# Optimization experiments

Hardware: AMD Instinct MI355X
Metric: run time of the kernel (lower is better)

## Reference

```python
import jax, jax.numpy as jnp
import numpy as np

N = 100000
D = 16          # input_dim
NUM_FILTERS = 8
NNZ = 1600000


def setup_inputs() -> dict:
    key = jax.random.key(0)
    k1, k2, k3, k4, k5 = jax.random.split(key, 5)
    x = jax.random.normal(k1, (N, D), dtype=jnp.float32)
    L_rows = jax.random.randint(k2, (NNZ,), 0, N, dtype=jnp.int64 if jax.config.jax_enable_x64 else jnp.int32).astype(jnp.int32)
    L_cols = jax.random.randint(k3, (NNZ,), 0, N, dtype=jnp.int32)
    L_v = jax.random.normal(k4, (NNZ,), dtype=jnp.float32)
    node_attr_eig = jax.random.uniform(k5, (N,), dtype=jnp.float32)
    return {"x": x, "L_rows": L_rows, "L_cols": L_cols, "L_v": L_v, "node_attr_eig": node_attr_eig}


def reference(x, L_rows, L_cols, L_v, node_attr_eig):
    n, d = x.shape
    f = NUM_FILTERS
    # exponents = 2 ** arange(num_filters + 1)
    exponents = (2 ** jnp.arange(f + 1)).astype(x.dtype)  # [F+1]
    # coeffs = x.T @ L  ==  (L.T @ x).T ; compute L.T @ x as [N, D]
    # (L.T @ x)[c] = sum over nnz entries (r, c): L_v * x[r]
    LTx = jax.ops.segment_sum(L_v[:, None] * x[L_rows], L_cols, num_segments=n)  # [N, D]
    # exponential eigenfilter bank: w = exp(-eig)^exponents, wavelet differences
    w = jnp.exp(-node_attr_eig)[:, None] ** exponents[None, :]  # [N, F+1]
    w_wav = w[:, :-1] - w[:, 1:]                                # [N, F]
    # g_eig = coeffs[..., None] * w_wav[None, ...] permuted to [N, D, F]
    g_eig = (LTx[:, :, None] * w_wav[:, None, :]).reshape(n, d * f)  # [N, D*F]
    # filtered = L @ g_eig : out[r] = sum over nnz (r, c): L_v * g_eig[c]
    out = jax.ops.segment_sum(L_v[:, None] * g_eig[L_cols], L_rows, num_segments=n)
    return out.reshape(n, d, f)
```

## Files before the change

kernel.cpp:

```cpp
#include <hip/hip_runtime.h>

#define N_NODES   100000
#define D_DIM     16
#define NFILT     8
#define KOUT      128
#define NNZ_CNT   1600000

#define CBITS     8
#define CROWS     256
#define NCB       ((N_NODES + CROWS - 1) / CROWS)
#define CAP       5120
#define EPB       4096
#define NBLKA     ((NNZ_CNT + EPB - 1) / EPB)

__device__ __forceinline__ uint f32_to_bf16_bits(float f) {
    uint u = __float_as_uint(f);
    uint r = (u + 0x7FFFu + ((u >> 16) & 1u)) >> 16;
    return r;
}

__global__ void wav_kernel(const float* __restrict__ eig, ushort* __restrict__ wavb) {
    int n = blockIdx.x * blockDim.x + threadIdx.x;
    if (n >= N_NODES) return;
    float cur = expf(-eig[n]);
    uint pk[4];
#pragma unroll
    for (int h = 0; h < 4; ++h) {
        float nx0 = cur * cur;
        float w0 = cur - nx0;
        float nx1 = nx0 * nx0;
        float w1 = nx0 - nx1;
        cur = nx1;
        pk[h] = f32_to_bf16_bits(w0) | (f32_to_bf16_bits(w1) << 16);
    }
    *(uint4*)(wavb + (size_t)n * NFILT) = make_uint4(pk[0], pk[1], pk[2], pk[3]);
}

__global__ __launch_bounds__(512) void binA_kernel(const int* __restrict__ keys,
                                                   const int* __restrict__ pays,
                                                   const float* __restrict__ v,
                                                   int* __restrict__ gcur,
                                                   int2* __restrict__ regA) {
    __shared__ int cnt[NCB];
    __shared__ int offb[NCB];
    __shared__ int gbase[NCB];
    __shared__ int sc[512];
    __shared__ int2 rec[EPB];
    int tid = threadIdx.x;
    int e0 = blockIdx.x * EPB;
    int nE = NNZ_CNT - e0; if (nE > EPB) nE = EPB;

    for (int i = tid; i < NCB; i += 512) cnt[i] = 0;
    __syncthreads();
    for (int i = tid; i < nE; i += 512)
        atomicAdd(&cnt[keys[e0 + i] >> CBITS], 1);
    __syncthreads();

    sc[tid] = (tid < NCB) ? cnt[tid] : 0;
    __syncthreads();
    for (int off = 1; off < 512; off <<= 1) {
        int t = (tid >= off) ? sc[tid - off] : 0;
        __syncthreads();
        sc[tid] += t;
        __syncthreads();
    }
    if (tid < NCB) {
        int cv = cnt[tid];
        int st = sc[tid] - cv;
        offb[tid] = st;
        gbase[tid] = cv ? atomicAdd(&gcur[tid], cv) : 0;
        cnt[tid] = st;
    }
    __syncthreads();

    for (int i = tid; i < nE; i += 512) {
        int k = keys[e0 + i], p = pays[e0 + i];
        float val = v[e0 + i];
        int b = k >> CBITS;
        int pos = atomicAdd(&cnt[b], 1);
        rec[pos] = make_int2(((k & (CROWS - 1)) << 17) | p, __float_as_int(val));
    }
    __syncthreads();

    int wv = tid >> 6, lane = tid & 63;
    for (int b = wv; b < NCB; b += 8) {
        int s = offb[b];
        int n = cnt[b] - s;
        size_t dst = (size_t)b * CAP + gbase[b];
        for (int i = lane; i < n; i += 64)
            regA[dst + i] = rec[s + i];
    }
}

__global__ __launch_bounds__(512) void binB_kernel(const int* __restrict__ gcur,
                                                   int2* __restrict__ regA,
                                                   int2* __restrict__ offs2) {
    __shared__ int2 rec[CAP];
    __shared__ int cnt[CROWS];
    __shared__ int sc[CROWS];
    int tid = threadIdx.x;
    int b = blockIdx.x;
    int nb = gcur[b]; if (nb > CAP) nb = CAP;
    size_t base = (size_t)b * CAP;

    if (tid < CROWS) cnt[tid] = 0;
    __syncthreads();
    for (int i = tid; i < nb; i += 512) {
        int2 r = regA[base + i];
        rec[i] = r;
        atomicAdd(&cnt[r.x >> 17], 1);
    }
    __syncthreads();

    int cv = (tid < CROWS) ? cnt[tid] : 0;
    if (tid < CROWS) sc[tid] = cv;
    __syncthreads();
    for (int off = 1; off < CROWS; off <<= 1) {
        int t = (tid < CROWS && tid >= off) ? sc[tid - off] : 0;
        __syncthreads();
        if (tid < CROWS) sc[tid] += t;
        __syncthreads();
    }
    if (tid < CROWS) {
        int st = sc[tid] - cv;
        int key = b * CROWS + tid;
        if (key < N_NODES)
            offs2[key] = make_int2((int)base + st, (int)base + st + cv);
        cnt[tid] = st;
    }
    __syncthreads();

    for (int i = tid; i < nb; i += 512) {
        int2 r = rec[i];
        int p = atomicAdd(&cnt[r.x >> 17], 1);
        regA[base + p] = make_int2(r.x & 0x1FFFF, r.y);
    }
}

__global__ __launch_bounds__(256) void gather1_kernel(const int2* __restrict__ offs2,
                                                      const int2* __restrict__ ep,
                                                      const float* __restrict__ x,
                                                      uint* __restrict__ LTxP) {
    int wave = (int)(((long long)blockIdx.x * blockDim.x + threadIdx.x) >> 6);
    if (wave >= N_NODES) return;
    int lane = threadIdx.x & 63;
    int c = wave;
    int d = lane & 15;
    int j = lane >> 4;
    int2 se = offs2[c];
    float acc = 0.f;
    for (int i = se.x + j; i < se.y; i += 4) {
        int2 e = ep[i];
        acc = fmaf(__int_as_float(e.y), x[(size_t)e.x * D_DIM + d], acc);
    }
    acc += __shfl_xor(acc, 16);
    acc += __shfl_xor(acc, 32);
    float hi = __shfl_down(acc, 8);
    if (lane < 8)
        LTxP[(size_t)c * NFILT + lane] = f32_to_bf16_bits(acc) | (f32_to_bf16_bits(hi) << 16);
}

__global__ __launch_bounds__(256) void gather2_kernel(const int2* __restrict__ offs2,
                                                      const int2* __restrict__ ep,
                                                      const uint* __restrict__ LTxP,
                                                      const ushort* __restrict__ wavb,
                                                      float* __restrict__ out) {
    int wave = (int)(((long long)blockIdx.x * blockDim.x + threadIdx.x) >> 6);
    if (wave >= N_NODES) return;
    int lane = threadIdx.x & 63;
    int r = wave;
    int d0 = lane >> 3;
    int f  = lane & 7;
    int2 se = offs2[r];
    int i = se.x, end = se.y;
    float acc0 = 0.f, acc1 = 0.f;
    for (; i + 4 <= end; i += 4) {
        int2 e0 = ep[i], e1 = ep[i + 1], e2 = ep[i + 2], e3 = ep[i + 3];
        uint l0 = LTxP[e0.x * NFILT + d0];
        uint l1 = LTxP[e1.x * NFILT + d0];
        uint l2 = LTxP[e2.x * NFILT + d0];
        uint l3 = LTxP[e3.x * NFILT + d0];
        uint w0 = wavb[e0.x * NFILT + f];
        uint w1 = wavb[e1.x * NFILT + f];
        uint w2 = wavb[e2.x * NFILT + f];
        uint w3 = wavb[e3.x * NFILT + f];
        float vw0 = __int_as_float(e0.y) * __uint_as_float(w0 << 16);
        float vw1 = __int_as_float(e1.y) * __uint_as_float(w1 << 16);
        float vw2 = __int_as_float(e2.y) * __uint_as_float(w2 << 16);
        float vw3 = __int_as_float(e3.y) * __uint_as_float(w3 << 16);
        acc0 = fmaf(vw0, __uint_as_float(l0 << 16), acc0);
        acc1 = fmaf(vw0, __uint_as_float(l0 & 0xFFFF0000u), acc1);
        acc0 = fmaf(vw1, __uint_as_float(l1 << 16), acc0);
        acc1 = fmaf(vw1, __uint_as_float(l1 & 0xFFFF0000u), acc1);
        acc0 = fmaf(vw2, __uint_as_float(l2 << 16), acc0);
        acc1 = fmaf(vw2, __uint_as_float(l2 & 0xFFFF0000u), acc1);
        acc0 = fmaf(vw3, __uint_as_float(l3 << 16), acc0);
        acc1 = fmaf(vw3, __uint_as_float(l3 & 0xFFFF0000u), acc1);
    }
    for (; i < end; ++i) {
        int2 e = ep[i];
        uint l = LTxP[e.x * NFILT + d0];
        uint w = wavb[e.x * NFILT + f];
        float vw = __int_as_float(e.y) * __uint_as_float(w << 16);
        acc0 = fmaf(vw, __uint_as_float(l << 16), acc0);
        acc1 = fmaf(vw, __uint_as_float(l & 0xFFFF0000u), acc1);
    }
    out[(size_t)r * KOUT + lane]      = acc0;
    out[(size_t)r * KOUT + 64 + lane] = acc1;
}

extern "C" void kernel_launch(void* const* d_in, const int* in_sizes, int n_in,
                              void* d_out, int out_size, void* d_ws, size_t ws_size,
                              hipStream_t stream) {
    const float* x      = (const float*)d_in[0];
    const int*   L_rows = (const int*)  d_in[1];
    const int*   L_cols = (const int*)  d_in[2];
    const float* L_v    = (const float*)d_in[3];
    const float* eig    = (const float*)d_in[4];
    float* out = (float*)d_out;

    uint*   LTxP  = (uint*)d_ws;
    ushort* wavb  = (ushort*)(LTxP + (size_t)N_NODES * NFILT);
    int2*   offs2 = (int2*)(wavb + (size_t)N_NODES * NFILT);
    int2*   regA  = offs2 + N_NODES;
    int*    gcur  = (int*)(regA + (size_t)NCB * CAP);
    int*    gcurB = gcur + NCB;

    hipMemsetAsync(gcur, 0, (size_t)2 * NCB * sizeof(int), stream);

    wav_kernel<<<(N_NODES + 255) / 256, 256, 0, stream>>>(eig, wavb);

    binA_kernel<<<NBLKA, 512, 0, stream>>>(L_cols, L_rows, L_v, gcurB, regA);
    binB_kernel<<<NCB, 512, 0, stream>>>(gcurB, regA, offs2);
    {
        long long threads = (long long)N_NODES * 64;
        gather1_kernel<<<(int)((threads + 255) / 256), 256, 0, stream>>>(offs2, regA, x, LTxP);
    }

    binA_kernel<<<NBLKA, 512, 0, stream>>>(L_rows, L_cols, L_v, gcur, regA);
    binB_kernel<<<NCB, 512, 0, stream>>>(gcur, regA, offs2);
    {
        long long threads = (long long)N_NODES * 64;
        gather2_kernel<<<(int)((threads + 255) / 256), 256, 0, stream>>>(offs2, regA, LTxP, wavb, out);
    }
}
```

Before: 283.5 us.

## Fuse bucket sort with gathers; accumulate first SpMM in LDS atomics

Drops the separate per-row sort kernels (binB) and the offsets array. The first product now accumulates L^T x directly into per-bucket shared-memory float atomics without sorting. The second product sorts each bucket's records in shared memory and then gathers from LDS. Bucket size is halved to 128 rows and the edges per block to 2048. binA now keeps its loaded keys in registers and writes out with a flat per-element loop. This saves two launches and a global read/write pass of the edge array. In exchange it adds shared-memory atomic contention, and the order of float summation becomes nondeterministic.

```diff
diff --git a/kernel.cpp b/kernel.cpp
--- a/kernel.cpp
+++ b/kernel.cpp
@@ -6,11 +6,11 @@
 #define KOUT      128
 #define NNZ_CNT   1600000
 
-#define CBITS     8
-#define CROWS     256
+#define CBITS     7
+#define CROWS     128
 #define NCB       ((N_NODES + CROWS - 1) / CROWS)
-#define CAP       5120
-#define EPB       4096
+#define CAP       2560
+#define EPB       2048
 #define NBLKA     ((NNZ_CNT + EPB - 1) / EPB)
 
 __device__ __forceinline__ uint f32_to_bf16_bits(float f) {
@@ -44,76 +44,131 @@
     __shared__ int cnt[NCB];
     __shared__ int offb[NCB];
     __shared__ int gbase[NCB];
-    __shared__ int sc[512];
+    __shared__ int sc[1024];
     __shared__ int2 rec[EPB];
+    __shared__ ushort rbk[EPB];
     int tid = threadIdx.x;
     int e0 = blockIdx.x * EPB;
     int nE = NNZ_CNT - e0; if (nE > EPB) nE = EPB;
 
     for (int i = tid; i < NCB; i += 512) cnt[i] = 0;
     __syncthreads();
-    for (int i = tid; i < nE; i += 512)
-        atomicAdd(&cnt[keys[e0 + i] >> CBITS], 1);
-    __syncthreads();
-
-    sc[tid] = (tid < NCB) ? cnt[tid] : 0;
-    __syncthreads();
-    for (int off = 1; off < 512; off <<= 1) {
-        int t = (tid >= off) ? sc[tid - off] : 0;
-        __syncthreads();
-        sc[tid] += t;
-        __syncthreads();
-    }
-    if (tid < NCB) {
-        int cv = cnt[tid];
-        int st = sc[tid] - cv;
-        offb[tid] = st;
-        gbase[tid] = cv ? atomicAdd(&gcur[tid], cv) : 0;
-        cnt[tid] = st;
+
+    int k_[4], p_[4], vb_[4];
+    int nk = 0;
+#pragma unroll
+    for (int kk = 0; kk < 4; ++kk) {
+        int i = tid + kk * 512;
+        if (i < nE) {
+            k_[kk] = keys[e0 + i];
+            p_[kk] = pays[e0 + i];
+            vb_[kk] = __float_as_int(v[e0 + i]);
+            nk = kk + 1;
+            atomicAdd(&cnt[k_[kk] >> CBITS], 1);
+        }
+    }
+    __syncthreads();
+
+    sc[tid]       = (tid < NCB) ? cnt[tid] : 0;
+    sc[tid + 512] = (tid + 512 < NCB) ? cnt[tid + 512] : 0;
+    __syncthreads();
+    for (int off = 1; off < 1024; off <<= 1) {
+        int t0 = (tid >= off) ? sc[tid - off] : 0;
+        int t1 = sc[tid + 512 - off];
+        __syncthreads();
+        sc[tid] += t0;
+        sc[tid + 512] += t1;
+        __syncthreads();
+    }
+    for (int bb = tid; bb < NCB; bb += 512) {
+        int cv = cnt[bb];
+        int st = sc[bb] - cv;
+        offb[bb] = st;
+        gbase[bb] = cv ? atomicAdd(&gcur[bb], cv) : 0;
+        cnt[bb] = st;
+    }
+    __syncthreads();
+
+    for (int kk = 0; kk < nk; ++kk) {
+        int b = k_[kk] >> CBITS;
+        int pos = atomicAdd(&cnt[b], 1);
+        rec[pos] = make_int2(((k_[kk] & (CROWS - 1)) << 17) | p_[kk], vb_[kk]);
+        rbk[pos] = (ushort)b;
     }
     __syncthreads();
 
     for (int i = tid; i < nE; i += 512) {
-        int k = keys[e0 + i], p = pays[e0 + i];
-        float val = v[e0 + i];
-        int b = k >> CBITS;
-        int pos = atomicAdd(&cnt[b], 1);
-        rec[pos] = make_int2(((k & (CROWS - 1)) << 17) | p, __float_as_int(val));
-    }
-    __syncthreads();
-
-    int wv = tid >> 6, lane = tid & 63;
-    for (int b = wv; b < NCB; b += 8) {
-        int s = offb[b];
-        int n = cnt[b] - s;
-        size_t dst = (size_t)b * CAP + gbase[b];
-        for (int i = lane; i < n; i += 64)
-            regA[dst + i] = rec[s + i];
-    }
-}
-
-__global__ __launch_bounds__(512) void binB_kernel(const int* __restrict__ gcur,
-                                                   int2* __restrict__ regA,
-                                                   int2* __restrict__ offs2) {
-    __shared__ int2 rec[CAP];
-    __shared__ int cnt[CROWS];
-    __shared__ int sc[CROWS];
+        int b = rbk[i];
+        regA[(size_t)b * CAP + gbase[b] + (i - offb[b])] = rec[i];
+    }
+}
+
+__global__ __launch_bounds__(512) void sortgather1_kernel(const int* __restrict__ gcur,
+                                                          const int2* __restrict__ regA,
+                                                          const float* __restrict__ x,
+                                                          uint* __restrict__ LTxP) {
+    __shared__ float acc[CROWS * D_DIM];
     int tid = threadIdx.x;
     int b = blockIdx.x;
     int nb = gcur[b]; if (nb > CAP) nb = CAP;
     size_t base = (size_t)b * CAP;
 
+    for (int t = tid; t < CROWS * D_DIM; t += 512) acc[t] = 0.f;
+    __syncthreads();
+
+    int wave = tid >> 6, lane = tid & 63;
+    int sub = lane >> 4;
+    int d = lane & 15;
+    for (int i = wave * 4 + sub; i < nb; i += 32) {
+        int2 e = regA[base + i];
+        int cl = e.x >> 17;
+        int r  = e.x & 0x1FFFF;
+        atomicAdd(&acc[cl * D_DIM + d], __int_as_float(e.y) * x[(size_t)r * D_DIM + d]);
+    }
+    __syncthreads();
+
+    for (int t = tid; t < CROWS * NFILT; t += 512) {
+        int cl = t >> 3, j = t & 7;
+        int c = b * CROWS + cl;
+        if (c < N_NODES)
+            LTxP[(size_t)c * NFILT + j] =
+                f32_to_bf16_bits(acc[cl * D_DIM + j]) |
+                (f32_to_bf16_bits(acc[cl * D_DIM + j + 8]) << 16);
+    }
+}
+
+__global__ __launch_bounds__(512) void sortgather2_kernel(const int* __restrict__ gcur,
+                                                          const int2* __restrict__ regA,
+                                                          const uint* __restrict__ LTxP,
+                                                          const ushort* __restrict__ wavb,
+                                                          float* __restrict__ out) {
+    __shared__ int2 rec[CAP];
+    __shared__ int cnt[CROWS];
+    __shared__ int sc[CROWS];
+    __shared__ int st[CROWS];
+    __shared__ int cur[CROWS];
+    int tid = threadIdx.x;
+    int b = blockIdx.x;
+    int nb = gcur[b]; if (nb > CAP) nb = CAP;
+    size_t base = (size_t)b * CAP;
+
+    int2 my[5]; int mrow[5];
+    int nk = 0;
     if (tid < CROWS) cnt[tid] = 0;
     __syncthreads();
-    for (int i = tid; i < nb; i += 512) {
-        int2 r = regA[base + i];
-        rec[i] = r;
-        atomicAdd(&cnt[r.x >> 17], 1);
-    }
-    __syncthreads();
-
-    int cv = (tid < CROWS) ? cnt[tid] : 0;
-    if (tid < CROWS) sc[tid] = cv;
+#pragma unroll
+    for (int k = 0; k < 5; ++k) {
+        int i = tid + k * 512;
+        if (i < nb) {
+            my[k] = regA[base + i];
+            mrow[k] = my[k].x >> 17;
+            nk = k + 1;
+            atomicAdd(&cnt[mrow[k]], 1);
+        }
+    }
+    __syncthreads();
+
+    if (tid < CROWS) sc[tid] = cnt[tid];
     __syncthreads();
     for (int off = 1; off < CROWS; off <<= 1) {
         int t = (tid < CROWS && tid >= off) ? sc[tid - off] : 0;
@@ -122,91 +177,60 @@
         __syncthreads();
     }
     if (tid < CROWS) {
-        int st = sc[tid] - cv;
-        int key = b * CROWS + tid;
-        if (key < N_NODES)
-            offs2[key] = make_int2((int)base + st, (int)base + st + cv);
-        cnt[tid] = st;
-    }
-    __syncthreads();
-
-    for (int i = tid; i < nb; i += 512) {
-        int2 r = rec[i];
-        int p = atomicAdd(&cnt[r.x >> 17], 1);
-        regA[base + p] = make_int2(r.x & 0x1FFFF, r.y);
-    }
-}
-
-__global__ __launch_bounds__(256) void gather1_kernel(const int2* __restrict__ offs2,
-                                                      const int2* __restrict__ ep,
-                                                      const float* __restrict__ x,
-                                                      uint* __restrict__ LTxP) {
-    int wave = (int)(((long long)blockIdx.x * blockDim.x + threadIdx.x) >> 6);
-    if (wave >= N_NODES) return;
-    int lane = threadIdx.x & 63;
-    int c = wave;
-    int d = lane & 15;
-    int j = lane >> 4;
-    int2 se = offs2[c];
-    float acc = 0.f;
-    for (int i = se.x + j; i < se.y; i += 4) {
-        int2 e = ep[i];
-        acc = fmaf(__int_as_float(e.y), x[(size_t)e.x * D_DIM + d], acc);
-    }
-    acc += __shfl_xor(acc, 16);
-    acc += __shfl_xor(acc, 32);
-    float hi = __shfl_down(acc, 8);
-    if (lane < 8)
-        LTxP[(size_t)c * NFILT + lane] = f32_to_bf16_bits(acc) | (f32_to_bf16_bits(hi) << 16);
-}
-
-__global__ __launch_bounds__(256) void gather2_kernel(const int2* __restrict__ offs2,
-                                                      const int2* __restrict__ ep,
-                                                      const uint* __restrict__ LTxP,
-                                                      const ushort* __restrict__ wavb,
-                                                      float* __restrict__ out) {
-    int wave = (int)(((long long)blockIdx.x * blockDim.x + threadIdx.x) >> 6);
-    if (wave >= N_NODES) return;
-    int lane = threadIdx.x & 63;
-    int r = wave;
+        int s = sc[tid] - cnt[tid];
+        st[tid] = s;
+        cur[tid] = s;
+    }
+    __syncthreads();
+
+    for (int k = 0; k < nk; ++k) {
+        int pos = atomicAdd(&cur[mrow[k]], 1);
+        rec[pos] = make_int2(my[k].x & 0x1FFFF, my[k].y);
+    }
+    __syncthreads();
+
+    int wave = tid >> 6, lane = tid & 63;
     int d0 = lane >> 3;
     int f  = lane & 7;
-    int2 se = offs2[r];
-    int i = se.x, end = se.y;
-    float acc0 = 0.f, acc1 = 0.f;
-    for (; i + 4 <= end; i += 4) {
-        int2 e0 = ep[i], e1 = ep[i + 1], e2 = ep[i + 2], e3 = ep[i + 3];
-        uint l0 = LTxP[e0.x * NFILT + d0];
-        uint l1 = LTxP[e1.x * NFILT + d0];
-        uint l2 = LTxP[e2.x * NFILT + d0];
-        uint l3 = LTxP[e3.x * NFILT + d0];
-        uint w0 = wavb[e0.x * NFILT + f];
-        uint w1 = wavb[e1.x * NFILT + f];
-        uint w2 = wavb[e2.x * NFILT + f];
-        uint w3 = wavb[e3.x * NFILT + f];
-        float vw0 = __int_as_float(e0.y) * __uint_as_float(w0 << 16);
-        float vw1 = __int_as_float(e1.y) * __uint_as_float(w1 << 16);
-        float vw2 = __int_as_float(e2.y) * __uint_as_float(w2 << 16);
-        float vw3 = __int_as_float(e3.y) * __uint_as_float(w3 << 16);
-        acc0 = fmaf(vw0, __uint_as_float(l0 << 16), acc0);
-        acc1 = fmaf(vw0, __uint_as_float(l0 & 0xFFFF0000u), acc1);
-        acc0 = fmaf(vw1, __uint_as_float(l1 << 16), acc0);
-        acc1 = fmaf(vw1, __uint_as_float(l1 & 0xFFFF0000u), acc1);
-        acc0 = fmaf(vw2, __uint_as_float(l2 << 16), acc0);
-        acc1 = fmaf(vw2, __uint_as_float(l2 & 0xFFFF0000u), acc1);
-        acc0 = fmaf(vw3, __uint_as_float(l3 << 16), acc0);
-        acc1 = fmaf(vw3, __uint_as_float(l3 & 0xFFFF0000u), acc1);
-    }
-    for (; i < end; ++i) {
-        int2 e = ep[i];
-        uint l = LTxP[e.x * NFILT + d0];
-        uint w = wavb[e.x * NFILT + f];
-        float vw = __int_as_float(e.y) * __uint_as_float(w << 16);
-        acc0 = fmaf(vw, __uint_as_float(l << 16), acc0);
-        acc1 = fmaf(vw, __uint_as_float(l & 0xFFFF0000u), acc1);
-    }
-    out[(size_t)r * KOUT + lane]      = acc0;
-    out[(size_t)r * KOUT + 64 + lane] = acc1;
+    for (int rl = wave; rl < CROWS; rl += 8) {
+        int row = b * CROWS + rl;
+        if (row >= N_NODES) continue;
+        int i = st[rl], end = st[rl] + cnt[rl];
+        float acc0 = 0.f, acc1 = 0.f;
+        for (; i + 4 <= end; i += 4) {
+            int2 e0 = rec[i], e1 = rec[i + 1], e2 = rec[i + 2], e3 = rec[i + 3];
+            uint l0 = LTxP[e0.x * NFILT + d0];
+            uint l1 = LTxP[e1.x * NFILT + d0];
+            uint l2 = LTxP[e2.x * NFILT + d0];
+            uint l3 = LTxP[e3.x * NFILT + d0];
+            uint w0 = wavb[e0.x * NFILT + f];
+            uint w1 = wavb[e1.x * NFILT + f];
+            uint w2 = wavb[e2.x * NFILT + f];
+            uint w3 = wavb[e3.x * NFILT + f];
+            float vw0 = __int_as_float(e0.y) * __uint_as_float(w0 << 16);
+            float vw1 = __int_as_float(e1.y) * __uint_as_float(w1 << 16);
+            float vw2 = __int_as_float(e2.y) * __uint_as_float(w2 << 16);
+            float vw3 = __int_as_float(e3.y) * __uint_as_float(w3 << 16);
+            acc0 = fmaf(vw0, __uint_as_float(l0 << 16), acc0);
+            acc1 = fmaf(vw0, __uint_as_float(l0 & 0xFFFF0000u), acc1);
+            acc0 = fmaf(vw1, __uint_as_float(l1 << 16), acc0);
+            acc1 = fmaf(vw1, __uint_as_float(l1 & 0xFFFF0000u), acc1);
+            acc0 = fmaf(vw2, __uint_as_float(l2 << 16), acc0);
+            acc1 = fmaf(vw2, __uint_as_float(l2 & 0xFFFF0000u), acc1);
+            acc0 = fmaf(vw3, __uint_as_float(l3 << 16), acc0);
+            acc1 = fmaf(vw3, __uint_as_float(l3 & 0xFFFF0000u), acc1);
+        }
+        for (; i < end; ++i) {
+            int2 e = rec[i];
+            uint l = LTxP[e.x * NFILT + d0];
+            uint w = wavb[e.x * NFILT + f];
+            float vw = __int_as_float(e.y) * __uint_as_float(w << 16);
+            acc0 = fmaf(vw, __uint_as_float(l << 16), acc0);
+            acc1 = fmaf(vw, __uint_as_float(l & 0xFFFF0000u), acc1);
+        }
+        out[(size_t)row * KOUT + lane]      = acc0;
+        out[(size_t)row * KOUT + 64 + lane] = acc1;
+    }
 }
 
 extern "C" void kernel_launch(void* const* d_in, const int* in_sizes, int n_in,
@@ -219,11 +243,10 @@
     const float* eig    = (const float*)d_in[4];
     float* out = (float*)d_out;
 
-    uint*   LTxP  = (uint*)d_ws;
-    ushort* wavb  = (ushort*)(LTxP + (size_t)N_NODES * NFILT);
-    int2*   offs2 = (int2*)(wavb + (size_t)N_NODES * NFILT);
-    int2*   regA  = offs2 + N_NODES;
-    int*    gcur  = (int*)(regA + (size_t)NCB * CAP);
+    uint*   LTxP = (uint*)d_ws;
+    ushort* wavb = (ushort*)(LTxP + (size_t)N_NODES * NFILT);
+    int2*   regA = (int2*)(wavb + (size_t)N_NODES * NFILT);
+    int*    gcur = (int*)(regA + (size_t)NCB * CAP);
     int*    gcurB = gcur + NCB;
 
     hipMemsetAsync(gcur, 0, (size_t)2 * NCB * sizeof(int), stream);
@@ -231,16 +254,8 @@
     wav_kernel<<<(N_NODES + 255) / 256, 256, 0, stream>>>(eig, wavb);
 
     binA_kernel<<<NBLKA, 512, 0, stream>>>(L_cols, L_rows, L_v, gcurB, regA);
-    binB_kernel<<<NCB, 512, 0, stream>>>(gcurB, regA, offs2);
-    {
-        long long threads = (long long)N_NODES * 64;
-        gather1_kernel<<<(int)((threads + 255) / 256), 256, 0, stream>>>(offs2, regA, x, LTxP);
-    }
+    sortgather1_kernel<<<NCB, 512, 0, stream>>>(gcurB, regA, x, LTxP);
 
     binA_kernel<<<NBLKA, 512, 0, stream>>>(L_rows, L_cols, L_v, gcur, regA);
-    binB_kernel<<<NCB, 512, 0, stream>>>(gcur, regA, offs2);
-    {
-        long long threads = (long long)N_NODES * 64;
-        gather2_kernel<<<(int)((threads + 255) / 256), 256, 0, stream>>>(offs2, regA, LTxP, wavb, out);
-    }
-}
+    sortgather2_kernel<<<NCB, 512, 0, stream>>>(gcur, regA, LTxP, wavb, out);
+}
```

Result: slower. 397.2 us (+40.1%).

## Replace block-local bucket sort with direct global-atomic binning into smaller buckets

Applied to the files above, without the earlier changes.

The shared-memory two-pass bucketing kernel (local histogram, scan, local scatter, coalesced copy-out) is replaced by a per-edge kernel that takes a global atomicAdd on the bucket counter and writes the record straight to its slot. Bucket width drops from 256 to 128 rows with capacity halved, which shrinks the per-bucket work in the second-stage sort. The intent is to remove the scan and barrier overhead of the first pass. The cost is about 1.6M global atomics on roughly 782 counters and scattered, uncoalesced writes. The output writes in the final gather also become nontemporal stores.

```diff
diff --git a/kernel.cpp b/kernel.cpp
--- a/kernel.cpp
+++ b/kernel.cpp
@@ -6,12 +6,10 @@
 #define KOUT      128
 #define NNZ_CNT   1600000
 
-#define CBITS     8
-#define CROWS     256
+#define CBITS     7
+#define CROWS     128
 #define NCB       ((N_NODES + CROWS - 1) / CROWS)
-#define CAP       5120
-#define EPB       4096
-#define NBLKA     ((NNZ_CNT + EPB - 1) / EPB)
+#define CAP       2560
 
 __device__ __forceinline__ uint f32_to_bf16_bits(float f) {
     uint u = __float_as_uint(f);
@@ -36,60 +34,21 @@
     *(uint4*)(wavb + (size_t)n * NFILT) = make_uint4(pk[0], pk[1], pk[2], pk[3]);
 }
 
-__global__ __launch_bounds__(512) void binA_kernel(const int* __restrict__ keys,
-                                                   const int* __restrict__ pays,
-                                                   const float* __restrict__ v,
-                                                   int* __restrict__ gcur,
-                                                   int2* __restrict__ regA) {
-    __shared__ int cnt[NCB];
-    __shared__ int offb[NCB];
-    __shared__ int gbase[NCB];
-    __shared__ int sc[512];
-    __shared__ int2 rec[EPB];
-    int tid = threadIdx.x;
-    int e0 = blockIdx.x * EPB;
-    int nE = NNZ_CNT - e0; if (nE > EPB) nE = EPB;
-
-    for (int i = tid; i < NCB; i += 512) cnt[i] = 0;
-    __syncthreads();
-    for (int i = tid; i < nE; i += 512)
-        atomicAdd(&cnt[keys[e0 + i] >> CBITS], 1);
-    __syncthreads();
-
-    sc[tid] = (tid < NCB) ? cnt[tid] : 0;
-    __syncthreads();
-    for (int off = 1; off < 512; off <<= 1) {
-        int t = (tid >= off) ? sc[tid - off] : 0;
-        __syncthreads();
-        sc[tid] += t;
-        __syncthreads();
-    }
-    if (tid < NCB) {
-        int cv = cnt[tid];
-        int st = sc[tid] - cv;
-        offb[tid] = st;
-        gbase[tid] = cv ? atomicAdd(&gcur[tid], cv) : 0;
-        cnt[tid] = st;
-    }
-    __syncthreads();
-
-    for (int i = tid; i < nE; i += 512) {
-        int k = keys[e0 + i], p = pays[e0 + i];
-        float val = v[e0 + i];
-        int b = k >> CBITS;
-        int pos = atomicAdd(&cnt[b], 1);
-        rec[pos] = make_int2(((k & (CROWS - 1)) << 17) | p, __float_as_int(val));
-    }
-    __syncthreads();
-
-    int wv = tid >> 6, lane = tid & 63;
-    for (int b = wv; b < NCB; b += 8) {
-        int s = offb[b];
-        int n = cnt[b] - s;
-        size_t dst = (size_t)b * CAP + gbase[b];
-        for (int i = lane; i < n; i += 64)
-            regA[dst + i] = rec[s + i];
-    }
+__global__ __launch_bounds__(256) void bin_direct_kernel(const int* __restrict__ keys,
+                                                         const int* __restrict__ pays,
+                                                         const float* __restrict__ v,
+                                                         int* __restrict__ gcur,
+                                                         int2* __restrict__ regA) {
+    int i = blockIdx.x * blockDim.x + threadIdx.x;
+    if (i >= NNZ_CNT) return;
+    int k = keys[i];
+    int p = pays[i];
+    float val = v[i];
+    int b = k >> CBITS;
+    int slot = atomicAdd(&gcur[b], 1);
+    if (slot < CAP)
+        regA[(size_t)b * CAP + slot] = make_int2(((k & (CROWS - 1)) << 17) | p,
+                                                 __float_as_int(val));
 }
 
 __global__ __launch_bounds__(512) void binB_kernel(const int* __restrict__ gcur,
@@ -205,8 +164,8 @@
         acc0 = fmaf(vw, __uint_as_float(l << 16), acc0);
         acc1 = fmaf(vw, __uint_as_float(l & 0xFFFF0000u), acc1);
     }
-    out[(size_t)r * KOUT + lane]      = acc0;
-    out[(size_t)r * KOUT + 64 + lane] = acc1;
+    __builtin_nontemporal_store(acc0, &out[(size_t)r * KOUT + lane]);
+    __builtin_nontemporal_store(acc1, &out[(size_t)r * KOUT + 64 + lane]);
 }
 
 extern "C" void kernel_launch(void* const* d_in, const int* in_sizes, int n_in,
@@ -230,14 +189,14 @@
 
     wav_kernel<<<(N_NODES + 255) / 256, 256, 0, stream>>>(eig, wavb);
 
-    binA_kernel<<<NBLKA, 512, 0, stream>>>(L_cols, L_rows, L_v, gcurB, regA);
+    bin_direct_kernel<<<(NNZ_CNT + 255) / 256, 256, 0, stream>>>(L_cols, L_rows, L_v, gcurB, regA);
     binB_kernel<<<NCB, 512, 0, stream>>>(gcurB, regA, offs2);
     {
         long long threads = (long long)N_NODES * 64;
         gather1_kernel<<<(int)((threads + 255) / 256), 256, 0, stream>>>(offs2, regA, x, LTxP);
     }
 
-    binA_kernel<<<NBLKA, 512, 0, stream>>>(L_rows, L_cols, L_v, gcur, regA);
+    bin_direct_kernel<<<(NNZ_CNT + 255) / 256, 256, 0, stream>>>(L_rows, L_cols, L_v, gcur, regA);
     binB_kernel<<<NCB, 512, 0, stream>>>(gcur, regA, offs2);
     {
         long long threads = (long long)N_NODES * 64;
```

New measurement: 977.1 us. +244.6%, slower.
